# Performance work log

Hardware: AMD Instinct MI355X
Metric: run time of the kernel (lower is better)

Reference implementation:

```python
import jax, jax.numpy as jnp
import numpy as np

DIM_IN = 25
H = 128        # num_neurons
P = 8000       # num_pixel
BS = 32
NEG_SLOPE = 0.01  # torch LeakyReLU default


def _leaky(x):
    return jnp.where(x >= 0, x, NEG_SLOPE * x)


def setup_inputs() -> dict:
    key = jax.random.key(0)
    ks = jax.random.split(key, 7)
    x = jax.random.normal(ks[0], (BS, DIM_IN), dtype=jnp.float32)
    # Stacked per-pixel MLP params (kaiming-ish scale to keep values sane)
    W1 = jax.random.normal(ks[1], (P, DIM_IN, H), dtype=jnp.float32) / np.sqrt(DIM_IN)
    b1 = jax.random.normal(ks[2], (P, H), dtype=jnp.float32) * 0.01
    W2 = jax.random.normal(ks[3], (P, H, H), dtype=jnp.float32) / np.sqrt(H)
    b2 = jax.random.normal(ks[4], (P, H), dtype=jnp.float32) * 0.01
    W3 = jax.random.normal(ks[5], (P, H), dtype=jnp.float32) / np.sqrt(H)
    b3 = jax.random.normal(ks[6], (P,), dtype=jnp.float32) * 0.01
    return {"x": x, "W1": W1, "b1": b1, "W2": W2, "b2": b2, "W3": W3, "b3": b3}


def reference(x, W1, b1, W2, b2, W3, b3):
    # h1: [bs, P, H] -- every pixel MLP sees the same x
    h1 = _leaky(jnp.einsum('bd,pdh->bph', x, W1) + b1[None])
    h2 = _leaky(jnp.einsum('bph,phk->bpk', h1, W2) + b2[None])
    # final Linear(num_neurons, 1) -> scalar per pixel -> y[bs, P]
    y = jnp.einsum('bph,ph->bp', h2, W3) + b3[None]
    return y
```

## Files before the change

kernel.cpp:

```cpp
#include <hip/hip_runtime.h>


constexpr int DIM_IN = 25;
constexpr int H      = 128;
constexpr int P      = 8000;
constexpr int BS     = 32;
constexpr float NEG  = 0.01f;

typedef short  short4v __attribute__((ext_vector_type(4)));
typedef short  short8v __attribute__((ext_vector_type(8)));
typedef float  f32x16  __attribute__((ext_vector_type(16)));

__device__ __forceinline__ float leaky(float v) { return v >= 0.f ? v : NEG * v; }

__device__ __forceinline__ short bf_rne(float f) {
    unsigned u = __builtin_bit_cast(unsigned, f);
    return (short)((u + 0x7fffu + ((u >> 16) & 1u)) >> 16);
}
__device__ __forceinline__ short bf_rna(float f) {
    unsigned u = __builtin_bit_cast(unsigned, f);
    return (short)((u + 0x8000u) >> 16);
}

#define STAGE_T(BUF, KT, HF) {                                                 \
    const float* gsrc_ = W2p + (size_t)(16 * (KT) + (t >> 4)) * H              \
                         + 64 * (HF) + ((t & 15) << 2);                        \
    float* dst_ = &w2t[BUF][0];                                                \
    _Pragma("unroll")                                                          \
    for (int i_ = 0; i_ < 4; ++i_)                                             \
        __builtin_amdgcn_global_load_lds(                                      \
            (const __attribute__((address_space(1))) unsigned*)(gsrc_ + (size_t)i_ * 4 * H), \
            (__attribute__((address_space(3))) unsigned*)(dst_ + i_ * 256),    \
            16, 0, 0); }

#define CONSUME_T(BUF, KT, HF) {                                               \
    const int ao_ = lo * 256 + 32 * (KT) + 16 * hi;                            \
    const short8v a_ = *reinterpret_cast<const short8v*>(                      \
        (const char*)h1b + (ao_ ^ ((lo & 7) << 4)));                           \
    const float* tb_ = &w2t[BUF][hi * 512 + lo];                               \
    _Pragma("unroll")                                                          \
    for (int n2_ = 0; n2_ < 2; ++n2_) {                                        \
        const float* col_ = tb_ + 32 * n2_;                                    \
        short8v bf_;                                                           \
        bf_[0] = bf_rna(col_[0]);   bf_[1] = bf_rna(col_[64]);                 \
        bf_[2] = bf_rna(col_[128]); bf_[3] = bf_rna(col_[192]);                \
        bf_[4] = bf_rna(col_[256]); bf_[5] = bf_rna(col_[320]);                \
        bf_[6] = bf_rna(col_[384]); bf_[7] = bf_rna(col_[448]);                \
        acc[2 * (HF) + n2_] = __builtin_amdgcn_mfma_f32_32x32x16_bf16(         \
            a_, bf_, acc[2 * (HF) + n2_], 0, 0, 0);                            \
    } }

__global__ __launch_bounds__(64, 2) void pixel_mlp_kernel(
    const float* __restrict__ x,
    const float* __restrict__ W1,
    const float* __restrict__ b1,
    const float* __restrict__ W2,
    const float* __restrict__ b2,
    const float* __restrict__ W3,
    const float* __restrict__ b3,
    float* __restrict__ y)
{
    const int p  = blockIdx.x;
    const int t  = threadIdx.x;
    const int cc = t & 15;
    const int gg = t >> 4;
    const int c0 = cc << 2;
    const int r0 = gg << 3;
    const int lo = t & 31;
    const int hi = t >> 5;

    __shared__ float sxT[DIM_IN][BS];
    __shared__ short h1b[BS][H];
    __shared__ float w2t[2][16 * 64];

    const float* W1p = W1 + (size_t)p * (DIM_IN * H);
    const float* W2p = W2 + (size_t)p * (H * H);

    const float4 b1l = *reinterpret_cast<const float4*>(b1 + (size_t)p * H + c0);
    const float4 b1h = *reinterpret_cast<const float4*>(b1 + (size_t)p * H + 64 + c0);
    float b2v[4], w3v[4];
    #pragma unroll
    for (int nb = 0; nb < 4; ++nb) {
        b2v[nb] = b2[(size_t)p * H + 32 * nb + lo];
        w3v[nb] = W3[(size_t)p * H + 32 * nb + lo];
    }
    const float b3s = b3[p];
    asm volatile("" ::: "memory");

    STAGE_T(0, 0, 0)
    STAGE_T(1, 0, 1)
    asm volatile("" ::: "memory");

    for (int i = t; i < DIM_IN * BS; i += 64)
        sxT[i >> 5][i & 31] = x[(i & 31) * DIM_IN + (i >> 5)];
    asm volatile("s_waitcnt lgkmcnt(0)" ::: "memory");

    float aL1[8][8];
    {
        const float bv[8] = {b1l.x, b1l.y, b1l.z, b1l.w, b1h.x, b1h.y, b1h.z, b1h.w};
        #pragma unroll
        for (int i = 0; i < 8; ++i)
            #pragma unroll
            for (int c = 0; c < 8; ++c)
                aL1[i][c] = bv[c];
    }
    #pragma unroll 5
    for (int d = 0; d < DIM_IN; ++d) {
        const float4 a0 = *reinterpret_cast<const float4*>(&sxT[d][r0]);
        const float4 a1 = *reinterpret_cast<const float4*>(&sxT[d][r0 + 4]);
        const float av[8] = {a0.x, a0.y, a0.z, a0.w, a1.x, a1.y, a1.z, a1.w};
        const float4 wl = *reinterpret_cast<const float4*>(W1p + d * H + c0);
        const float4 wh = *reinterpret_cast<const float4*>(W1p + d * H + 64 + c0);
        const float wv[8] = {wl.x, wl.y, wl.z, wl.w, wh.x, wh.y, wh.z, wh.w};
        #pragma unroll
        for (int i = 0; i < 8; ++i)
            #pragma unroll
            for (int c = 0; c < 8; ++c)
                aL1[i][c] += av[i] * wv[c];
    }

    #pragma unroll
    for (int i = 0; i < 8; ++i) {
        short4v lov, hiv;
        lov[0] = bf_rne(leaky(aL1[i][0])); lov[1] = bf_rne(leaky(aL1[i][1]));
        lov[2] = bf_rne(leaky(aL1[i][2])); lov[3] = bf_rne(leaky(aL1[i][3]));
        hiv[0] = bf_rne(leaky(aL1[i][4])); hiv[1] = bf_rne(leaky(aL1[i][5]));
        hiv[2] = bf_rne(leaky(aL1[i][6])); hiv[3] = bf_rne(leaky(aL1[i][7]));
        const int ro = (r0 + i) * 256;
        const int sz = ((r0 + i) & 7) << 4;
        *reinterpret_cast<short4v*>((char*)h1b + ((ro + 8 * cc) ^ sz))       = lov;
        *reinterpret_cast<short4v*>((char*)h1b + ((ro + 128 + 8 * cc) ^ sz)) = hiv;
    }
    asm volatile("s_waitcnt lgkmcnt(0)" ::: "memory");
    __builtin_amdgcn_sched_barrier(0);

    f32x16 acc[4];
    #pragma unroll
    for (int nb = 0; nb < 4; ++nb)
        acc[nb] = (f32x16)(0.f);

    #pragma unroll 1
    for (int kt = 0; kt < 7; ++kt) {
        asm volatile("s_waitcnt vmcnt(4)" ::: "memory");
        CONSUME_T(0, kt, 0)
        asm volatile("s_waitcnt lgkmcnt(0)" ::: "memory");
        STAGE_T(0, kt + 1, 0)
        asm volatile("s_waitcnt vmcnt(4)" ::: "memory");
        CONSUME_T(1, kt, 1)
        asm volatile("s_waitcnt lgkmcnt(0)" ::: "memory");
        STAGE_T(1, kt + 1, 1)
    }
    asm volatile("s_waitcnt vmcnt(4)" ::: "memory");
    CONSUME_T(0, 7, 0)
    asm volatile("s_waitcnt vmcnt(0)" ::: "memory");
    CONSUME_T(1, 7, 1)

    float s[16];
    #pragma unroll
    for (int reg = 0; reg < 16; ++reg) {
        float acc_s = 0.f;
        #pragma unroll
        for (int nb = 0; nb < 4; ++nb)
            acc_s += leaky(acc[nb][reg] + b2v[nb]) * w3v[nb];
        s[reg] = acc_s;
    }
    #pragma unroll
    for (int m = 16; m >= 1; m >>= 1) {
        #pragma unroll
        for (int reg = 0; reg < 16; ++reg)
            s[reg] += __shfl_xor(s[reg], m);
    }
    if (lo == 0) {
        #pragma unroll
        for (int reg = 0; reg < 16; ++reg) {
            const int r = (reg & 3) + 8 * (reg >> 2) + 4 * hi;
            y[(size_t)r * P + p] = s[reg] + b3s;
        }
    }
}

extern "C" void kernel_launch(void* const* d_in, const int* in_sizes, int n_in,
                              void* d_out, int out_size, void* d_ws, size_t ws_size,
                              hipStream_t stream) {
    const float* x  = (const float*)d_in[0];
    const float* W1 = (const float*)d_in[1];
    const float* b1 = (const float*)d_in[2];
    const float* W2 = (const float*)d_in[3];
    const float* b2 = (const float*)d_in[4];
    const float* W3 = (const float*)d_in[5];
    const float* b3 = (const float*)d_in[6];
    float* y = (float*)d_out;

    pixel_mlp_kernel<<<dim3(P), dim3(64), 0, stream>>>(x, W1, b1, W2, b2, W3, b3, y);
}
```

Baseline: 130.9 us.

## Stream W1 through LDS double buffer and pipeline into W2 prefetch

Layer-1 weights are now staged into the shared double buffer with async global-to-LDS loads in 8-row tiles, instead of being read directly from global memory inside the FMA loop. The last W1 row is loaded into registers up front. The first W2 tiles are issued while layer-1 compute is still finishing, so the W2 stream starts earlier, and the buffer roles in the W2 loop are swapped to match. The aim is to hide the W1 load latency and the W2 pipeline start-up, at the cost of more manual waitcnt choreography and extra LDS reads during layer 1.

```diff
diff --git a/kernel.cpp b/kernel.cpp
--- a/kernel.cpp
+++ b/kernel.cpp
@@ -22,22 +22,49 @@
     return (short)((u + 0x8000u) >> 16);
 }
 
-#define STAGE_T(BUF, KT, HF) {                                                 \
-    const float* gsrc_ = W2p + (size_t)(16 * (KT) + (t >> 4)) * H              \
-                         + 64 * (HF) + ((t & 15) << 2);                        \
-    float* dst_ = &w2t[BUF][0];                                                \
+#define STAGE_W1(BUF, T8) {                                                    \
+    const float* g_ = W1p + (size_t)(8 * (T8)) * H + (t << 2);                 \
+    float* d_ = &w12t[BUF][0];                                                 \
     _Pragma("unroll")                                                          \
     for (int i_ = 0; i_ < 4; ++i_)                                             \
         __builtin_amdgcn_global_load_lds(                                      \
-            (const __attribute__((address_space(1))) unsigned*)(gsrc_ + (size_t)i_ * 4 * H), \
-            (__attribute__((address_space(3))) unsigned*)(dst_ + i_ * 256),    \
+            (const __attribute__((address_space(1))) unsigned*)(g_ + i_ * 256),\
+            (__attribute__((address_space(3))) unsigned*)(d_ + i_ * 256),      \
             16, 0, 0); }
+
+#define STAGE_T(BUF, KT, HF) {                                                 \
+    const float* g_ = W2p + (size_t)(16 * (KT) + (t >> 4)) * H                 \
+                      + 64 * (HF) + ((t & 15) << 2);                           \
+    float* d_ = &w12t[BUF][0];                                                 \
+    _Pragma("unroll")                                                          \
+    for (int i_ = 0; i_ < 4; ++i_)                                             \
+        __builtin_amdgcn_global_load_lds(                                      \
+            (const __attribute__((address_space(1))) unsigned*)(g_ + (size_t)i_ * 4 * H), \
+            (__attribute__((address_space(3))) unsigned*)(d_ + i_ * 256),      \
+            16, 0, 0); }
+
+#define L1_CONSUME(BUF, T8) {                                                  \
+    _Pragma("unroll")                                                          \
+    for (int dd_ = 0; dd_ < 8; ++dd_) {                                        \
+        const int d_ = 8 * (T8) + dd_;                                         \
+        const float4 a0_ = *reinterpret_cast<const float4*>(&sxT[d_][r0]);     \
+        const float4 a1_ = *reinterpret_cast<const float4*>(&sxT[d_][r0 + 4]); \
+        const float4 wl_ = *reinterpret_cast<const float4*>(&w12t[BUF][dd_ * H + c0]); \
+        const float4 wh_ = *reinterpret_cast<const float4*>(&w12t[BUF][dd_ * H + 64 + c0]); \
+        const float av_[8] = {a0_.x, a0_.y, a0_.z, a0_.w, a1_.x, a1_.y, a1_.z, a1_.w}; \
+        const float wv_[8] = {wl_.x, wl_.y, wl_.z, wl_.w, wh_.x, wh_.y, wh_.z, wh_.w}; \
+        _Pragma("unroll")                                                      \
+        for (int i_ = 0; i_ < 8; ++i_)                                         \
+            _Pragma("unroll")                                                  \
+            for (int c_ = 0; c_ < 8; ++c_)                                     \
+                aL1[i_][c_] += av_[i_] * wv_[c_];                              \
+    } }
 
 #define CONSUME_T(BUF, KT, HF) {                                               \
     const int ao_ = lo * 256 + 32 * (KT) + 16 * hi;                            \
     const short8v a_ = *reinterpret_cast<const short8v*>(                      \
         (const char*)h1b + (ao_ ^ ((lo & 7) << 4)));                           \
-    const float* tb_ = &w2t[BUF][hi * 512 + lo];                               \
+    const float* tb_ = &w12t[BUF][hi * 512 + lo];                              \
     _Pragma("unroll")                                                          \
     for (int n2_ = 0; n2_ < 2; ++n2_) {                                        \
         const float* col_ = tb_ + 32 * n2_;                                    \
@@ -71,13 +98,15 @@
 
     __shared__ float sxT[DIM_IN][BS];
     __shared__ short h1b[BS][H];
-    __shared__ float w2t[2][16 * 64];
+    __shared__ float w12t[2][16 * 64];
 
     const float* W1p = W1 + (size_t)p * (DIM_IN * H);
     const float* W2p = W2 + (size_t)p * (H * H);
 
-    const float4 b1l = *reinterpret_cast<const float4*>(b1 + (size_t)p * H + c0);
-    const float4 b1h = *reinterpret_cast<const float4*>(b1 + (size_t)p * H + 64 + c0);
+    const float4 b1l  = *reinterpret_cast<const float4*>(b1 + (size_t)p * H + c0);
+    const float4 b1h  = *reinterpret_cast<const float4*>(b1 + (size_t)p * H + 64 + c0);
+    const float4 w24l = *reinterpret_cast<const float4*>(W1p + 24 * H + c0);
+    const float4 w24h = *reinterpret_cast<const float4*>(W1p + 24 * H + 64 + c0);
     float b2v[4], w3v[4];
     #pragma unroll
     for (int nb = 0; nb < 4; ++nb) {
@@ -87,8 +116,8 @@
     const float b3s = b3[p];
     asm volatile("" ::: "memory");
 
-    STAGE_T(0, 0, 0)
-    STAGE_T(1, 0, 1)
+    STAGE_W1(0, 0)
+    STAGE_W1(1, 1)
     asm volatile("" ::: "memory");
 
     for (int i = t; i < DIM_IN * BS; i += 64)
@@ -104,20 +133,31 @@
             for (int c = 0; c < 8; ++c)
                 aL1[i][c] = bv[c];
     }
-    #pragma unroll 5
-    for (int d = 0; d < DIM_IN; ++d) {
-        const float4 a0 = *reinterpret_cast<const float4*>(&sxT[d][r0]);
-        const float4 a1 = *reinterpret_cast<const float4*>(&sxT[d][r0 + 4]);
+
+    asm volatile("s_waitcnt vmcnt(4)" ::: "memory");
+    L1_CONSUME(0, 0)
+    asm volatile("s_waitcnt lgkmcnt(0)" ::: "memory");
+    STAGE_W1(0, 2)
+    asm volatile("s_waitcnt vmcnt(4)" ::: "memory");
+    L1_CONSUME(1, 1)
+    asm volatile("s_waitcnt lgkmcnt(0)" ::: "memory");
+    STAGE_T(1, 0, 0)
+    asm volatile("s_waitcnt vmcnt(4)" ::: "memory");
+    L1_CONSUME(0, 2)
+    {
+        const float4 a0 = *reinterpret_cast<const float4*>(&sxT[24][r0]);
+        const float4 a1 = *reinterpret_cast<const float4*>(&sxT[24][r0 + 4]);
         const float av[8] = {a0.x, a0.y, a0.z, a0.w, a1.x, a1.y, a1.z, a1.w};
-        const float4 wl = *reinterpret_cast<const float4*>(W1p + d * H + c0);
-        const float4 wh = *reinterpret_cast<const float4*>(W1p + d * H + 64 + c0);
-        const float wv[8] = {wl.x, wl.y, wl.z, wl.w, wh.x, wh.y, wh.z, wh.w};
+        const float wv[8] = {w24l.x, w24l.y, w24l.z, w24l.w,
+                             w24h.x, w24h.y, w24h.z, w24h.w};
         #pragma unroll
         for (int i = 0; i < 8; ++i)
             #pragma unroll
             for (int c = 0; c < 8; ++c)
                 aL1[i][c] += av[i] * wv[c];
     }
+    asm volatile("s_waitcnt lgkmcnt(0)" ::: "memory");
+    STAGE_T(0, 0, 1)
 
     #pragma unroll
     for (int i = 0; i < 8; ++i) {
@@ -142,18 +182,18 @@
     #pragma unroll 1
     for (int kt = 0; kt < 7; ++kt) {
         asm volatile("s_waitcnt vmcnt(4)" ::: "memory");
-        CONSUME_T(0, kt, 0)
+        CONSUME_T(1, kt, 0)
         asm volatile("s_waitcnt lgkmcnt(0)" ::: "memory");
-        STAGE_T(0, kt + 1, 0)
+        STAGE_T(1, kt + 1, 0)
         asm volatile("s_waitcnt vmcnt(4)" ::: "memory");
-        CONSUME_T(1, kt, 1)
+        CONSUME_T(0, kt, 1)
         asm volatile("s_waitcnt lgkmcnt(0)" ::: "memory");
-        STAGE_T(1, kt + 1, 1)
-    }
-    asm volatile("s_waitcnt vmcnt(4)" ::: "memory");
-    CONSUME_T(0, 7, 0)
+        STAGE_T(0, kt + 1, 1)
+    }
+    asm volatile("s_waitcnt vmcnt(4)" ::: "memory");
+    CONSUME_T(1, 7, 0)
     asm volatile("s_waitcnt vmcnt(0)" ::: "memory");
-    CONSUME_T(1, 7, 1)
+    CONSUME_T(0, 7, 1)
 
     float s[16];
     #pragma unroll
```

New measurement: 131.4 us. Within noise of the previous version (+0.4%).
